# Kernel optimization log

Hardware: AMD Instinct MI355X
Metric: run time of the kernel (lower is better)

Reference implementation:

```python
import jax, jax.numpy as jnp
import numpy as np

N_NODES = 50000
N_EDGES = 800000
DIM = 64


def _param(key, shape, scale):
    return jax.random.normal(key, shape, dtype=jnp.float32) * scale


def setup_inputs() -> dict:
    key = jax.random.key(0)
    ks = jax.random.split(key, 20)
    s = 1.0 / np.sqrt(DIM)
    x = jax.random.normal(ks[0], (N_NODES, DIM), dtype=jnp.float32)
    weights = jax.random.uniform(ks[1], (6,), dtype=jnp.float32)
    edge_index = jax.random.randint(ks[2], (2, N_EDGES), 0, N_NODES, dtype=jnp.int64)
    return {
        "x": x,
        "weights": weights,
        # mlp
        "W_mlp": _param(ks[3], (DIM, DIM), s), "b_mlp": jnp.zeros((DIM,), jnp.float32),
        # sage (mean aggregator): lin_l on neighbor mean, lin_r on self
        "Wl_sage": _param(ks[4], (DIM, DIM), s), "Wr_sage": _param(ks[5], (DIM, DIM), s),
        "b_sage": jnp.zeros((DIM,), jnp.float32),
        # gcn
        "W_gcn": _param(ks[6], (DIM, DIM), s), "b_gcn": jnp.zeros((DIM,), jnp.float32),
        # gat (single head)
        "W_gat": _param(ks[7], (DIM, DIM), s),
        "a_src": _param(ks[8], (DIM,), s), "a_dst": _param(ks[9], (DIM,), s),
        "b_gat": jnp.zeros((DIM,), jnp.float32),
        # chebconv K=3
        "W_cheb": _param(ks[10], (3, DIM, DIM), s), "b_cheb": jnp.zeros((DIM,), jnp.float32),
        # gin (eps=0, nn = Linear)
        "W_gin": _param(ks[11], (DIM, DIM), s), "b_gin": jnp.zeros((DIM,), jnp.float32),
        "edge_index": edge_index,
    }


def _mixed_forward(x, weights, W_mlp, b_mlp, Wl_sage, Wr_sage, b_sage,
                   W_gcn, b_gcn, W_gat, a_src, a_dst, b_gat,
                   W_cheb, b_cheb, W_gin, b_gin, edge_index):
    N = x.shape[0]
    src, dst = edge_index[0], edge_index[1]
    seg_sum = lambda v, idx: jax.ops.segment_sum(v, idx, num_segments=N)

    deg = seg_sum(jnp.ones(src.shape[0], x.dtype), dst)  # in-degree [N]
    nsum = seg_sum(x[src], dst)                           # sum of neighbor feats [N, D]

    # --- mlp (graph-free) ---
    o_mlp = x @ W_mlp + b_mlp

    # --- sage, mean aggregation ---
    nmean = nsum / jnp.maximum(deg, 1.0)[:, None]
    o_sage = nmean @ Wl_sage + x @ Wr_sage + b_sage

    # --- gcn with self loops: D'^{-1/2} (A+I) D'^{-1/2} X W ---
    dinv = jax.lax.rsqrt(deg + 1.0)
    xw = x @ W_gcn
    norm_e = dinv[src] * dinv[dst]
    o_gcn = seg_sum(norm_e[:, None] * xw[src], dst) + xw * (dinv * dinv)[:, None] + b_gcn

    # --- gat, single head, self loops appended, leaky_relu(0.2) scoring ---
    h = x @ W_gat
    el, er = h @ a_src, h @ a_dst
    loop = jnp.arange(N, dtype=src.dtype)
    src2 = jnp.concatenate([src, loop])
    dst2 = jnp.concatenate([dst, loop])
    e = jax.nn.leaky_relu(el[src2] + er[dst2], 0.2)
    m = jax.ops.segment_max(e, dst2, num_segments=N)
    p = jnp.exp(e - m[dst2])
    z = jax.ops.segment_sum(p, dst2, num_segments=N)
    alpha = p / (z[dst2] + 1e-16)
    o_gat = jax.ops.segment_sum(alpha[:, None] * h[src2], dst2, num_segments=N) + b_gat

    # --- cheb K=3, lambda_max=2: L_hat = L_norm - I = -A_norm ---
    dinv_c = jax.lax.rsqrt(jnp.maximum(deg, 1.0))
    nrm = dinv_c[src] * dinv_c[dst]
    prop = lambda t: seg_sum(nrm[:, None] * t[src], dst)
    T0 = x
    T1 = -prop(T0)
    T2 = -2.0 * prop(T1) - T0
    o_cheb = T0 @ W_cheb[0] + T1 @ W_cheb[1] + T2 @ W_cheb[2] + b_cheb

    # --- gin, eps=0, nn = Linear ---
    o_gin = (x + nsum) @ W_gin + b_gin

    outs = (o_mlp, o_sage, o_gcn, o_gat, o_cheb, o_gin)
    res = jnp.zeros_like(o_mlp)
    for k, o in enumerate(outs):
        res = res + weights[k] * jax.nn.elu(o)
    return res


def reference(x, weights, W_mlp, b_mlp, Wl_sage, Wr_sage, b_sage,
              W_gcn, b_gcn, W_gat, a_src, a_dst, b_gat,
              W_cheb, b_cheb, W_gin, b_gin, edge_index):
    return _mixed_forward(x, weights, W_mlp, b_mlp, Wl_sage, Wr_sage, b_sage,
                          W_gcn, b_gcn, W_gat, a_src, a_dst, b_gat,
                          W_cheb, b_cheb, W_gin, b_gin, edge_index)
```

## Files before the change

### kernel.cpp

```cpp
#include <hip/hip_runtime.h>
#include <cstdint>
#include <cstddef>

#define NN 50000
#define NE 800000
#define CAP 96
#define NSEG 8
#define SEGW 6250

constexpr size_t O_CNT   = 0;
constexpr size_t O_SLOT  = 50048;
constexpr size_t O_NODAL = O_SLOT + (size_t)NN*CAP;
constexpr size_t O_VA    = O_NODAL + 200000;
constexpr size_t O_VB    = O_VA + 64;
constexpr size_t O_XB    = O_VB + 64;
constexpr size_t O_NSB   = O_XB + 1600032;
constexpr size_t O_T1B   = O_NSB + 1600000;
constexpr size_t O_V1B   = O_T1B + 1600032;
constexpr size_t O_GB    = O_V1B + 1600000;
constexpr size_t O_UB    = O_GB  + 1600000;
constexpr size_t O_WPK   = O_UB  + 1600000;

typedef __attribute__((ext_vector_type(8))) short short8;
typedef __attribute__((ext_vector_type(4))) float f32x4;

__device__ __forceinline__ float leaky02(float v){ return v >= 0.f ? v : 0.2f*v; }
__device__ __forceinline__ float eluf(float v){ return v > 0.f ? v : (__expf(v) - 1.f); }

__device__ __forceinline__ void lds_fence(){
  asm volatile("s_waitcnt lgkmcnt(0)" ::: "memory");
}

__device__ __forceinline__ unsigned short f2bf(float f){
  unsigned u = __float_as_uint(f);
  unsigned r = (u + 0x7FFFu + ((u >> 16) & 1u)) >> 16;
  return (unsigned short)r;
}
__device__ __forceinline__ float bf2f(unsigned short b){
  return __uint_as_float(((unsigned)b) << 16);
}
__device__ __forceinline__ unsigned pack2(unsigned short lo, unsigned short hi){
  return (unsigned)lo | ((unsigned)hi << 16);
}

__global__ __launch_bounds__(256) void k_scatter(
    const int* __restrict__ src, const int* __restrict__ dst,
    int* __restrict__ cnt, unsigned short* __restrict__ slot,
    const float* __restrict__ W_mlp, const float* __restrict__ Wr,
    const float* __restrict__ W_cheb, const float* __restrict__ W_gin,
    const float* __restrict__ Wl, const float* __restrict__ W_gcn,
    const float* __restrict__ W_gat,
    const float* __restrict__ a_src, const float* __restrict__ a_dst,
    const float4* __restrict__ x4,
    float* __restrict__ va, float* __restrict__ vb,
    unsigned short* __restrict__ wpk,
    ushort4* __restrict__ xb4, ushort4* __restrict__ t1b4){
  int b = blockIdx.x;
  int seg = b & (NSEG-1);
  int e = (b >> 3)*256 + threadIdx.x;
  if (e < NE){
    int d = dst[e];
    if (d / SEGW == seg){
      int s = src[e];
      int pos = atomicAdd(&cnt[d], 1);
      if (pos < CAP) slot[(size_t)d*CAP + pos] = (unsigned short)s;
    }
  }
  if (b == 0){
    int k = threadIdx.x;
    if (k < 64){
      float sa = 0.f, sb = 0.f;
      for (int j = 0; j < 64; ++j){
        float w = W_gat[k*64 + j];
        sa = fmaf(w, a_src[j], sa);
        sb = fmaf(w, a_dst[j], sb);
      }
      va[k] = sa; vb[k] = sb;
    }
  } else if (b <= 9){
    int w = b - 1;
    const float* s; const float* sub = nullptr;
    switch (w){
      case 0: s = W_mlp; break;
      case 1: s = Wr; break;
      case 2: s = W_cheb; sub = W_cheb + 8192; break;
      case 3: s = W_gin; break;
      case 4: s = Wl; break;
      case 5: s = W_cheb + 4096; break;
      case 6: s = W_cheb + 8192; break;
      case 7: s = W_gcn; break;
      default: s = W_gat; break;
    }
    for (int ee = threadIdx.x; ee < 4096; ee += 256){
      int k = ee >> 6, n = ee & 63;
      float f = s[ee];
      if (sub) f -= sub[ee];
      wpk[(size_t)w*4096 + (size_t)n*64 + k] = f2bf(f);
    }
  } else if (b < 3136){
    int i = (b - 10)*256 + threadIdx.x;
    if (i < NN*16){
      float4 v = x4[i];
      ushort4 o;
      o.x = f2bf(v.x); o.y = f2bf(v.y); o.z = f2bf(v.z); o.w = f2bf(v.w);
      xb4[i] = o;
    } else if (i < (NN+1)*16){
      ushort4 z; z.x = 0; z.y = 0; z.z = 0; z.w = 0;
      xb4[i] = z;
      t1b4[i] = z;
    }
  }
}

__global__ __launch_bounds__(256) void k_nodal(const float* __restrict__ x,
    const int* __restrict__ cnt, const float* __restrict__ va, const float* __restrict__ vb,
    float4* __restrict__ nodal){
  int tid = threadIdx.x;
  int li = tid & 15;
  int row = blockIdx.x*16 + (tid >> 4);
  if (row >= NN) return;
  float4 hv = *(const float4*)&x[(size_t)row*64 + li*4];
  float4 av = *(const float4*)&va[li*4];
  float4 bv = *(const float4*)&vb[li*4];
  float ps = hv.x*av.x + hv.y*av.y + hv.z*av.z + hv.w*av.w;
  float pd = hv.x*bv.x + hv.y*bv.y + hv.z*bv.z + hv.w*bv.w;
  #pragma unroll
  for (int o = 1; o < 16; o <<= 1){ ps += __shfl_xor(ps, o); pd += __shfl_xor(pd, o); }
  if (li == 0){
    float c = (float)cnt[row];
    float dinv  = rsqrtf(c + 1.f);
    float dinvc = rsqrtf(fmaxf(c, 1.f));
    nodal[row] = make_float4(dinvc, dinv, ps, pd);
  }
}

__global__ __launch_bounds__(256) void k_aggA(const float* __restrict__ x,
    const unsigned short* __restrict__ xb,
    const int* __restrict__ cnt, const unsigned short* __restrict__ slot,
    const float4* __restrict__ nodal,
    unsigned* __restrict__ nsb2, unsigned* __restrict__ t1b2,
    unsigned* __restrict__ v1b2, unsigned* __restrict__ gb2){
  __shared__ float4 sW[4][64];
  int wid  = threadIdx.x >> 6;
  int lane = threadIdx.x & 63;
  int node = blockIdx.x*4 + wid;
  if (node >= NN) return;
  int c = min(cnt[node], CAP);
  const unsigned short* sl = slot + (size_t)node*CAP;
  float4 nn = nodal[node];
  float ern = nn.w;
  int half = lane >> 5, hl = lane & 31;
  float a0e=0.f,a0o=0.f,a1e=0.f,a1o=0.f,a2e=0.f,a2o=0.f,a3e=0.f,a3o=0.f, zl=0.f;
  for (int base = 0; base < c; base += 64){
    int rem = min(64, c - base);
    bool act = lane < rem;
    int s = act ? (int)sl[base+lane] : NN;
    float4 ns = act ? nodal[s] : make_float4(0.f,0.f,0.f,0.f);
    float p = act ? __expf(fminf(leaky02(ns.z + ern), 60.f)) : 0.f;
    zl += p;
    sW[wid][lane] = make_float4(__int_as_float(s), ns.x, ns.y, p);
    lds_fence();
    for (int j = 0; j < rem; j += 8){
      float4 w[4]; unsigned uv[4];
      #pragma unroll
      for (int q2 = 0; q2 < 4; ++q2){
        w[q2] = sW[wid][j + 2*q2 + half];
        int sb = __float_as_int(w[q2].x);
        sb = ((unsigned)sb <= (unsigned)NN) ? sb : NN;
        uv[q2] = *(const unsigned*)&xb[(size_t)sb*64 + 2*hl];
      }
      #pragma unroll
      for (int q2 = 0; q2 < 4; ++q2){
        float lo = __uint_as_float(uv[q2] << 16);
        float hi = __uint_as_float(uv[q2] & 0xffff0000u);
        a0e += lo;                       a0o += hi;
        a1e = fmaf(w[q2].y, lo, a1e);    a1o = fmaf(w[q2].y, hi, a1o);
        a2e = fmaf(w[q2].z, lo, a2e);    a2o = fmaf(w[q2].z, hi, a2o);
        a3e = fmaf(w[q2].w, lo, a3e);    a3o = fmaf(w[q2].w, hi, a3o);
      }
    }
    lds_fence();
  }
  a0e += __shfl_xor(a0e, 32); a0o += __shfl_xor(a0o, 32);
  a1e += __shfl_xor(a1e, 32); a1o += __shfl_xor(a1o, 32);
  a2e += __shfl_xor(a2e, 32); a2o += __shfl_xor(a2o, 32);
  a3e += __shfl_xor(a3e, 32); a3o += __shfl_xor(a3o, 32);
  #pragma unroll
  for (int o = 32; o > 0; o >>= 1) zl += __shfl_xor(zl, o);
  float2 xs = *(const float2*)&x[(size_t)node*64 + 2*hl];
  float p_self = __expf(fminf(leaky02(nn.z + nn.w), 60.f));
  float rz = 1.f / (zl + p_self + 1e-16f);
  size_t off2 = (size_t)node*32 + hl;
  if (half == 0){
    nsb2[off2] = pack2(f2bf(a0e), f2bf(a0o));
    t1b2[off2] = pack2(f2bf(-nn.x*a1e), f2bf(-nn.x*a1o));
  } else {
    v1b2[off2] = pack2(f2bf(nn.y*a2e + nn.y*nn.y*xs.x), f2bf(nn.y*a2o + nn.y*nn.y*xs.y));
    gb2[off2]  = pack2(f2bf((a3e + p_self*xs.x)*rz), f2bf((a3o + p_self*xs.y)*rz));
  }
}

__global__ __launch_bounds__(256) void k_aggB(const unsigned short* __restrict__ t1b,
    const int* __restrict__ cnt, const unsigned short* __restrict__ slot,
    const float4* __restrict__ nodal, unsigned* __restrict__ ub2){
  __shared__ float2 sW[4][64];
  int wid  = threadIdx.x >> 6;
  int lane = threadIdx.x & 63;
  int node = blockIdx.x*4 + wid;
  if (node >= NN) return;
  int c = min(cnt[node], CAP);
  const unsigned short* sl = slot + (size_t)node*CAP;
  const float* nf = (const float*)nodal;
  int half = lane >> 5, hl = lane & 31;
  float ae = 0.f, ao = 0.f;
  for (int base = 0; base < c; base += 64){
    int rem = min(64, c - base);
    bool act = lane < rem;
    int s = act ? (int)sl[base+lane] : NN;
    float dc = act ? nf[(size_t)s*4] : 0.f;
    sW[wid][lane] = make_float2(__int_as_float(s), dc);
    lds_fence();
    for (int j = 0; j < rem; j += 8){
      float2 w[4]; unsigned uv[4];
      #pragma unroll
      for (int q2 = 0; q2 < 4; ++q2){
        w[q2] = sW[wid][j + 2*q2 + half];
        int sb = __float_as_int(w[q2].x);
        sb = ((unsigned)sb <= (unsigned)NN) ? sb : NN;
        uv[q2] = *(const unsigned*)&t1b[(size_t)sb*64 + 2*hl];
      }
      #pragma unroll
      for (int q2 = 0; q2 < 4; ++q2){
        float lo = __uint_as_float(uv[q2] << 16);
        float hi = __uint_as_float(uv[q2] & 0xffff0000u);
        ae = fmaf(w[q2].y, lo, ae);
        ao = fmaf(w[q2].y, hi, ao);
      }
    }
    lds_fence();
  }
  ae += __shfl_xor(ae, 32);
  ao += __shfl_xor(ao, 32);
  if (half == 0){
    float sc = -2.f * nodal[node].x;
    ub2[(size_t)node*32 + hl] = pack2(f2bf(sc*ae), f2bf(sc*ao));
  }
}

__global__ __launch_bounds__(64) void k_epi(
    const float* __restrict__ wts,
    const float* __restrict__ b_mlp, const float* __restrict__ b_sage,
    const float* __restrict__ b_gcn, const float* __restrict__ b_gat,
    const float* __restrict__ b_cheb, const float* __restrict__ b_gin,
    const float4* __restrict__ nodal, const unsigned short* __restrict__ wpk,
    const unsigned short* __restrict__ xb, const unsigned short* __restrict__ nsb,
    const unsigned short* __restrict__ t1b, const unsigned short* __restrict__ v1b,
    const unsigned short* __restrict__ gb, const unsigned short* __restrict__ ub,
    float* __restrict__ out){
  const int lane = threadIdx.x;
  const int ml   = lane & 15;
  const int q    = lane >> 4;
  const int rowbase = blockIdx.x*16;
  const float w0 = wts[0], w1 = wts[1], w2 = wts[2], w3 = wts[3], w4 = wts[4], w5 = wts[5];
  const float* nod = (const float*)nodal;

  short8 ah0, ah1;

  auto loadA = [&](const unsigned short* __restrict__ src){
    const unsigned short* p = src + (size_t)(rowbase + ml)*64 + q*8;
    ah0 = *(const short8*)p;
    ah1 = *(const short8*)(p + 32);
  };
  auto group = [&](int w, f32x4 acc[4]){
    const unsigned short* base = wpk + (size_t)w*4096;
    #pragma unroll
    for (int nt = 0; nt < 4; ++nt){
      const unsigned short* bp = base + (size_t)(nt*16 + ml)*64;
      short8 b0 = *(const short8*)(bp + q*8);
      short8 b1 = *(const short8*)(bp + 32 + q*8);
      acc[nt] = __builtin_amdgcn_mfma_f32_16x16x32_bf16(ah0, b0, acc[nt], 0, 0, 0);
      acc[nt] = __builtin_amdgcn_mfma_f32_16x16x32_bf16(ah1, b1, acc[nt], 0, 0, 0);
    }
  };

  f32x4 res[4];
  #pragma unroll
  for (int i = 0; i < 4; ++i) res[i] = (f32x4){0.f,0.f,0.f,0.f};

  auto emit = [&](const f32x4 acc[4], const float* __restrict__ bias, float wk){
    #pragma unroll
    for (int nt = 0; nt < 4; ++nt){
      float b = bias[nt*16 + ml];
      #pragma unroll
      for (int r = 0; r < 4; ++r) res[nt][r] += wk * eluf(acc[nt][r] + b);
    }
  };

  f32x4 t[4], accC[4], accWr[4], accG[4];

  loadA(v1b);
  #pragma unroll
  for (int i=0;i<4;++i) t[i] = (f32x4){0.f,0.f,0.f,0.f};
  group(7, t); emit(t, b_gcn, w2);
  loadA(gb);
  #pragma unroll
  for (int i=0;i<4;++i) t[i] = (f32x4){0.f,0.f,0.f,0.f};
  group(8, t); emit(t, b_gat, w3);
  loadA(ub);
  #pragma unroll
  for (int i=0;i<4;++i) accC[i] = (f32x4){0.f,0.f,0.f,0.f};
  group(6, accC);
  loadA(t1b);
  group(5, accC);
  loadA(xb);
  #pragma unroll
  for (int i=0;i<4;++i) t[i] = (f32x4){0.f,0.f,0.f,0.f};
  group(0, t); emit(t, b_mlp, w0);
  #pragma unroll
  for (int i=0;i<4;++i) accWr[i] = (f32x4){0.f,0.f,0.f,0.f};
  group(1, accWr);
  group(2, accC); emit(accC, b_cheb, w4);
  #pragma unroll
  for (int i=0;i<4;++i) accG[i] = (f32x4){0.f,0.f,0.f,0.f};
  group(3, accG);
  loadA(nsb);
  group(3, accG); emit(accG, b_gin, w5);
  #pragma unroll
  for (int i=0;i<4;++i) t[i] = (f32x4){0.f,0.f,0.f,0.f};
  group(4, t);
  #pragma unroll
  for (int nt = 0; nt < 4; ++nt){
    float b = b_sage[nt*16 + ml];
    #pragma unroll
    for (int r = 0; r < 4; ++r){
      int row = rowbase + q*4 + r;
      float dc = nod[(size_t)row*4];
      float invd = dc*dc;
      res[nt][r] += w1 * eluf(invd*t[nt][r] + accWr[nt][r] + b);
    }
  }
  #pragma unroll
  for (int nt = 0; nt < 4; ++nt){
    int col = nt*16 + ml;
    #pragma unroll
    for (int r = 0; r < 4; ++r){
      int row = rowbase + q*4 + r;
      out[(size_t)row*64 + col] = res[nt][r];
    }
  }
}

extern "C" void kernel_launch(void* const* d_in, const int* in_sizes, int n_in,
                              void* d_out, int out_size, void* d_ws, size_t ws_size,
                              hipStream_t stream){
  const float* x      = (const float*)d_in[0];
  const float* wts    = (const float*)d_in[1];
  const float* W_mlp  = (const float*)d_in[2];
  const float* b_mlp  = (const float*)d_in[3];
  const float* Wl     = (const float*)d_in[4];
  const float* Wr     = (const float*)d_in[5];
  const float* b_sage = (const float*)d_in[6];
  const float* W_gcn  = (const float*)d_in[7];
  const float* b_gcn  = (const float*)d_in[8];
  const float* W_gat  = (const float*)d_in[9];
  const float* a_src  = (const float*)d_in[10];
  const float* a_dst  = (const float*)d_in[11];
  const float* b_gat  = (const float*)d_in[12];
  const float* W_cheb = (const float*)d_in[13];
  const float* b_cheb = (const float*)d_in[14];
  const float* W_gin  = (const float*)d_in[15];
  const float* b_gin  = (const float*)d_in[16];
  const int*   ei     = (const int*)d_in[17];

  float* wsf  = (float*)d_ws;
  int*  cnt   = (int*)d_ws;
  unsigned short* slot = (unsigned short*)(wsf + O_SLOT);
  float4* nodal = (float4*)(wsf + O_NODAL);
  float* va   = wsf + O_VA;
  float* vb   = wsf + O_VB;
  unsigned short* xbu = (unsigned short*)(wsf + O_XB);
  unsigned short* nsb = (unsigned short*)(wsf + O_NSB);
  unsigned short* t1b = (unsigned short*)(wsf + O_T1B);
  unsigned short* v1b = (unsigned short*)(wsf + O_V1B);
  unsigned short* gb  = (unsigned short*)(wsf + O_GB);
  unsigned short* ub  = (unsigned short*)(wsf + O_UB);
  unsigned short* wpk = (unsigned short*)(wsf + O_WPK);
  float* out  = (float*)d_out;

  hipMemsetAsync(cnt, 0, NN*sizeof(int), stream);
  k_scatter <<<25000,256, 0, stream>>>(ei, ei + NE, cnt, slot,
                                       W_mlp, Wr, W_cheb, W_gin, Wl, W_gcn, W_gat,
                                       a_src, a_dst, (const float4*)x,
                                       va, vb, wpk, (ushort4*)xbu, (ushort4*)t1b);
  k_nodal   <<<3125, 256, 0, stream>>>(x, cnt, va, vb, nodal);
  k_aggA    <<<12500,256, 0, stream>>>(x, xbu, cnt, slot, nodal,
                                       (unsigned*)nsb, (unsigned*)t1b,
                                       (unsigned*)v1b, (unsigned*)gb);
  k_aggB    <<<12500,256, 0, stream>>>(t1b, cnt, slot, nodal, (unsigned*)ub);
  k_epi     <<<3125,  64, 0, stream>>>(wts, b_mlp, b_sage, b_gcn, b_gat, b_cheb, b_gin,
                                       nodal, wpk, xbu, nsb, t1b, v1b, gb, ub, out);
}
```

Baseline: 225.5 us.

## Vectorize edge scatter, pack per-edge weights as bf16, cache combined slot list

The scatter kernel now reads four edges per thread via int4 loads and launches a quarter as many blocks. aggA packs source index and per-edge coefficients into bf16 pairs in LDS, unrolls the gather to 8 per iteration, and writes a combined (src, dinv_c) word per edge to a new buffer. aggB reads that buffer directly instead of re-gathering nodal data for each neighbour. The aim is to cut index loads, random nodal gathers and LDS traffic, at the cost of bf16 rounding of edge weights and extra global writes in aggA.

```diff
diff --git a/kernel.cpp b/kernel.cpp
--- a/kernel.cpp
+++ b/kernel.cpp
@@ -20,6 +20,7 @@
 constexpr size_t O_GB    = O_V1B + 1600000;
 constexpr size_t O_UB    = O_GB  + 1600000;
 constexpr size_t O_WPK   = O_UB  + 1600000;
+constexpr size_t O_CMB   = O_WPK + 18432;
 
 typedef __attribute__((ext_vector_type(8))) short short8;
 typedef __attribute__((ext_vector_type(4))) float f32x4;
@@ -44,7 +45,7 @@
 }
 
 __global__ __launch_bounds__(256) void k_scatter(
-    const int* __restrict__ src, const int* __restrict__ dst,
+    const int4* __restrict__ src4, const int4* __restrict__ dst4,
     int* __restrict__ cnt, unsigned short* __restrict__ slot,
     const float* __restrict__ W_mlp, const float* __restrict__ Wr,
     const float* __restrict__ W_cheb, const float* __restrict__ W_gin,
@@ -57,14 +58,15 @@
     ushort4* __restrict__ xb4, ushort4* __restrict__ t1b4){
   int b = blockIdx.x;
   int seg = b & (NSEG-1);
-  int e = (b >> 3)*256 + threadIdx.x;
-  if (e < NE){
-    int d = dst[e];
-    if (d / SEGW == seg){
-      int s = src[e];
-      int pos = atomicAdd(&cnt[d], 1);
-      if (pos < CAP) slot[(size_t)d*CAP + pos] = (unsigned short)s;
-    }
+  int i4 = (b >> 3)*256 + threadIdx.x;
+  if (i4 < NE/4){
+    int4 d = dst4[i4];
+    int4 s = src4[i4];
+    int pos;
+    if (d.x / SEGW == seg){ pos = atomicAdd(&cnt[d.x], 1); if (pos < CAP) slot[(size_t)d.x*CAP + pos] = (unsigned short)s.x; }
+    if (d.y / SEGW == seg){ pos = atomicAdd(&cnt[d.y], 1); if (pos < CAP) slot[(size_t)d.y*CAP + pos] = (unsigned short)s.y; }
+    if (d.z / SEGW == seg){ pos = atomicAdd(&cnt[d.z], 1); if (pos < CAP) slot[(size_t)d.z*CAP + pos] = (unsigned short)s.z; }
+    if (d.w / SEGW == seg){ pos = atomicAdd(&cnt[d.w], 1); if (pos < CAP) slot[(size_t)d.w*CAP + pos] = (unsigned short)s.w; }
   }
   if (b == 0){
     int k = threadIdx.x;
@@ -139,8 +141,9 @@
     const int* __restrict__ cnt, const unsigned short* __restrict__ slot,
     const float4* __restrict__ nodal,
     unsigned* __restrict__ nsb2, unsigned* __restrict__ t1b2,
-    unsigned* __restrict__ v1b2, unsigned* __restrict__ gb2){
-  __shared__ float4 sW[4][64];
+    unsigned* __restrict__ v1b2, unsigned* __restrict__ gb2,
+    unsigned* __restrict__ cmb){
+  __shared__ uint2 sU[4][64];
   int wid  = threadIdx.x >> 6;
   int lane = threadIdx.x & 63;
   int node = blockIdx.x*4 + wid;
@@ -157,26 +160,32 @@
     int s = act ? (int)sl[base+lane] : NN;
     float4 ns = act ? nodal[s] : make_float4(0.f,0.f,0.f,0.f);
     float p = act ? __expf(fminf(leaky02(ns.z + ern), 60.f)) : 0.f;
+    p = bf2f(f2bf(p));
     zl += p;
-    sW[wid][lane] = make_float4(__int_as_float(s), ns.x, ns.y, p);
+    if (act) cmb[(size_t)node*CAP + base + lane] = pack2((unsigned short)s, f2bf(ns.x));
+    sU[wid][lane] = make_uint2(pack2((unsigned short)s, f2bf(p)),
+                               pack2(f2bf(ns.x), f2bf(ns.y)));
     lds_fence();
-    for (int j = 0; j < rem; j += 8){
-      float4 w[4]; unsigned uv[4];
+    for (int j = 0; j < rem; j += 16){
+      uint2 w[8]; unsigned uv[8];
       #pragma unroll
-      for (int q2 = 0; q2 < 4; ++q2){
-        w[q2] = sW[wid][j + 2*q2 + half];
-        int sb = __float_as_int(w[q2].x);
-        sb = ((unsigned)sb <= (unsigned)NN) ? sb : NN;
+      for (int q2 = 0; q2 < 8; ++q2){
+        w[q2] = sU[wid][j + 2*q2 + half];
+        unsigned sb = w[q2].x & 0xffffu;
+        sb = (sb <= (unsigned)NN) ? sb : NN;
         uv[q2] = *(const unsigned*)&xb[(size_t)sb*64 + 2*hl];
       }
       #pragma unroll
-      for (int q2 = 0; q2 < 4; ++q2){
+      for (int q2 = 0; q2 < 8; ++q2){
+        float pb  = bf2f((unsigned short)(w[q2].x >> 16));
+        float dcb = bf2f((unsigned short)(w[q2].y & 0xffffu));
+        float dvb = bf2f((unsigned short)(w[q2].y >> 16));
         float lo = __uint_as_float(uv[q2] << 16);
         float hi = __uint_as_float(uv[q2] & 0xffff0000u);
         a0e += lo;                       a0o += hi;
-        a1e = fmaf(w[q2].y, lo, a1e);    a1o = fmaf(w[q2].y, hi, a1o);
-        a2e = fmaf(w[q2].z, lo, a2e);    a2o = fmaf(w[q2].z, hi, a2o);
-        a3e = fmaf(w[q2].w, lo, a3e);    a3o = fmaf(w[q2].w, hi, a3o);
+        a1e = fmaf(dcb, lo, a1e);        a1o = fmaf(dcb, hi, a1o);
+        a2e = fmaf(dvb, lo, a2e);        a2o = fmaf(dvb, hi, a2o);
+        a3e = fmaf(pb,  lo, a3e);        a3o = fmaf(pb,  hi, a3o);
       }
     }
     lds_fence();
@@ -201,40 +210,38 @@
 }
 
 __global__ __launch_bounds__(256) void k_aggB(const unsigned short* __restrict__ t1b,
-    const int* __restrict__ cnt, const unsigned short* __restrict__ slot,
+    const int* __restrict__ cnt, const unsigned* __restrict__ cmb,
     const float4* __restrict__ nodal, unsigned* __restrict__ ub2){
-  __shared__ float2 sW[4][64];
+  __shared__ unsigned sB[4][64];
   int wid  = threadIdx.x >> 6;
   int lane = threadIdx.x & 63;
   int node = blockIdx.x*4 + wid;
   if (node >= NN) return;
   int c = min(cnt[node], CAP);
-  const unsigned short* sl = slot + (size_t)node*CAP;
-  const float* nf = (const float*)nodal;
   int half = lane >> 5, hl = lane & 31;
   float ae = 0.f, ao = 0.f;
   for (int base = 0; base < c; base += 64){
     int rem = min(64, c - base);
     bool act = lane < rem;
-    int s = act ? (int)sl[base+lane] : NN;
-    float dc = act ? nf[(size_t)s*4] : 0.f;
-    sW[wid][lane] = make_float2(__int_as_float(s), dc);
+    unsigned cw = act ? cmb[(size_t)node*CAP + base + lane] : pack2(NN, 0);
+    sB[wid][lane] = cw;
     lds_fence();
-    for (int j = 0; j < rem; j += 8){
-      float2 w[4]; unsigned uv[4];
+    for (int j = 0; j < rem; j += 16){
+      unsigned w[8]; unsigned uv[8];
       #pragma unroll
-      for (int q2 = 0; q2 < 4; ++q2){
-        w[q2] = sW[wid][j + 2*q2 + half];
-        int sb = __float_as_int(w[q2].x);
-        sb = ((unsigned)sb <= (unsigned)NN) ? sb : NN;
+      for (int q2 = 0; q2 < 8; ++q2){
+        w[q2] = sB[wid][j + 2*q2 + half];
+        unsigned sb = w[q2] & 0xffffu;
+        sb = (sb <= (unsigned)NN) ? sb : NN;
         uv[q2] = *(const unsigned*)&t1b[(size_t)sb*64 + 2*hl];
       }
       #pragma unroll
-      for (int q2 = 0; q2 < 4; ++q2){
+      for (int q2 = 0; q2 < 8; ++q2){
+        float dc = bf2f((unsigned short)(w[q2] >> 16));
         float lo = __uint_as_float(uv[q2] << 16);
         float hi = __uint_as_float(uv[q2] & 0xffff0000u);
-        ae = fmaf(w[q2].y, lo, ae);
-        ao = fmaf(w[q2].y, hi, ao);
+        ae = fmaf(dc, lo, ae);
+        ao = fmaf(dc, hi, ao);
       }
     }
     lds_fence();
@@ -385,18 +392,19 @@
   unsigned short* gb  = (unsigned short*)(wsf + O_GB);
   unsigned short* ub  = (unsigned short*)(wsf + O_UB);
   unsigned short* wpk = (unsigned short*)(wsf + O_WPK);
+  unsigned* cmb = (unsigned*)(wsf + O_CMB);
   float* out  = (float*)d_out;
 
   hipMemsetAsync(cnt, 0, NN*sizeof(int), stream);
-  k_scatter <<<25000,256, 0, stream>>>(ei, ei + NE, cnt, slot,
+  k_scatter <<<6256, 256, 0, stream>>>((const int4*)ei, (const int4*)(ei + NE), cnt, slot,
                                        W_mlp, Wr, W_cheb, W_gin, Wl, W_gcn, W_gat,
                                        a_src, a_dst, (const float4*)x,
                                        va, vb, wpk, (ushort4*)xbu, (ushort4*)t1b);
   k_nodal   <<<3125, 256, 0, stream>>>(x, cnt, va, vb, nodal);
   k_aggA    <<<12500,256, 0, stream>>>(x, xbu, cnt, slot, nodal,
                                        (unsigned*)nsb, (unsigned*)t1b,
-                                       (unsigned*)v1b, (unsigned*)gb);
-  k_aggB    <<<12500,256, 0, stream>>>(t1b, cnt, slot, nodal, (unsigned*)ub);
+                                       (unsigned*)v1b, (unsigned*)gb, cmb);
+  k_aggB    <<<12500,256, 0, stream>>>(t1b, cnt, cmb, nodal, (unsigned*)ub);
   k_epi     <<<3125,  64, 0, stream>>>(wts, b_mlp, b_sage, b_gcn, b_gat, b_cheb, b_gin,
                                        nodal, wpk, xbu, nsb, t1b, v1b, gb, ub, out);
 }
```

Result: slower. 232.7 us (+3.2%).
